# Kernel tuning notes

Hardware: AMD Instinct MI355X
Metric: run time of the kernel (lower is better)

## Reference

```python
import jax, jax.numpy as jnp
import numpy as np


def gat(feat_src, feat_dst, src, dst, W, al, ar, b):
    # DGL GATConv in eval mode: shared fc for src/dst, additive attention,
    # leaky_relu(0.2), edge-softmax per destination node, elu activation, bias.
    H, D = al.shape
    nd = feat_dst.shape[0]
    hs = (feat_src @ W).reshape(-1, H, D)  # [Ns,H,D]
    hd = (feat_dst @ W).reshape(-1, H, D)  # [Nd,H,D]
    el = (hs * al).sum(-1)  # [Ns,H]
    er = (hd * ar).sum(-1)  # [Nd,H]
    e = jax.nn.leaky_relu(el[src] + er[dst], 0.2)  # [E,H]
    m = jax.lax.stop_gradient(jax.ops.segment_max(e, dst, num_segments=nd))
    a = jnp.exp(e - m[dst])
    s = jax.ops.segment_sum(a, dst, num_segments=nd)
    den = s[dst]
    alpha = a / jnp.where(den == 0, 1.0, den)  # allow_zero_in_degree
    rst = jax.ops.segment_sum(alpha[:, :, None] * hs[src], dst, num_segments=nd)
    return jax.nn.elu(rst + b.reshape(H, D))  # [Nd,H,D]


def setup_inputs():
    key = jax.random.key(0)
    ks = jax.random.split(key, 40)
    NP, NQ, NK, NA = 50000, 20000, 30000, 5000
    EM, EQ, EK, EA = 1600000, 200000, 200000, 100000
    IN, ATT, HID, H, OUT = 128, 64, 32, 4, 1000
    w = lambda k, sh: jax.random.normal(k, sh, jnp.float32) * 0.05
    ri = lambda k, e, n: jax.random.randint(k, (e,), 0, n, dtype=jnp.int32)
    d = dict(
        hp=jax.random.normal(ks[0], (NP, IN), jnp.float32),
        hq=jax.random.normal(ks[1], (NQ, ATT), jnp.float32),
        hk=jax.random.normal(ks[2], (NK, ATT), jnp.float32),
        ha=jax.random.normal(ks[3], (NA, ATT), jnp.float32),
        meta_src=ri(ks[4], EM, NP), meta_dst=ri(ks[5], EM, NP),
        q_src=ri(ks[6], EQ, NQ), q_dst=ri(ks[7], EQ, NP),
        k_src=ri(ks[8], EK, NK), k_dst=ri(ks[9], EK, NP),
        a_src=ri(ks[10], EA, NA), a_dst=ri(ks[11], EA, NP),
        W0=w(ks[12], (IN, H * HID)), al0=w(ks[13], (H, HID)), ar0=w(ks[14], (H, HID)), b0=jnp.zeros((H * HID,), jnp.float32),
        W1=w(ks[15], (H * HID, H * HID)), al1=w(ks[16], (H, HID)), ar1=w(ks[17], (H, HID)), b1=jnp.zeros((H * HID,), jnp.float32),
        Wq=w(ks[18], (64, H * 128)), alq=w(ks[19], (H, 128)), arq=w(ks[20], (H, 128)), bq=jnp.zeros((H * 128,), jnp.float32),
        Wkw=w(ks[21], (64, H * 128)), alkw=w(ks[22], (H, 128)), arkw=w(ks[23], (H, 128)), bkw=jnp.zeros((H * 128,), jnp.float32),
        Watt=w(ks[24], (64, H * 128)), alatt=w(ks[25], (H, 128)), aratt=w(ks[26], (H, 128)), batt=jnp.zeros((H * 128,), jnp.float32),
        Wpnn_a=w(ks[27], (IN, 64)), Wpn_a=w(ks[28], (ATT, 64)),
        Wpnn=w(ks[29], (H * HID, 64)), Wpn=w(ks[30], (H * 128, 64)),
        Wpred=w(ks[31], (256, OUT)), bpred=jnp.zeros((OUT,), jnp.float32),
    )
    return d


def reference(hp, hq, hk, ha, meta_src, meta_dst, q_src, q_dst, k_src, k_dst, a_src, a_dst, W0, al0, ar0, b0, W1, al1, ar1, b1, Wq, alq, arq, bq, Wkw, alkw, arkw, bkw, Watt, alatt, aratt, batt, Wpnn_a, Wpn_a, Wpnn, Wpn, Wpred, bpred):
    NP = hp.shape[0]
    # two pnn_layers over the single used metapath graph (index 1 is skipped in the original)
    h = gat(hp, hp, meta_src, meta_dst, W0, al0, ar0, b0).reshape(NP, -1)  # [NP,128]
    h = gat(h, h, meta_src, meta_dst, W1, al1, ar1, b1).reshape(NP, -1)    # [NP,128]
    hpd = hp @ Wpnn_a  # proj_pnn_a(hp_cache) -> dst features for bipartite GATs
    oq = gat(hq @ Wpn_a, hpd, q_src, q_dst, Wq, alq, arq, bq).reshape(NP, -1)      # [NP,512]
    ok = gat(hk @ Wpn_a, hpd, k_src, k_dst, Wkw, alkw, arkw, bkw).reshape(NP, -1)  # [NP,512]
    oa = gat(ha @ Wpn_a, hpd, a_src, a_dst, Watt, alatt, aratt, batt).reshape(NP, -1)  # [NP,512]
    hcat = jnp.concatenate([h @ Wpnn, oq @ Wpn, ok @ Wpn, oa @ Wpn], axis=1)  # [NP,256]
    return hcat @ Wpred + bpred
```

## Files before the change

### kernel.cpp

```cpp
#include <hip/hip_runtime.h>
#include <hip/hip_bf16.h>
#include <math.h>
#include <stdint.h>

typedef __attribute__((ext_vector_type(8))) short bh8;
typedef __attribute__((ext_vector_type(4))) float f32x4;

#define AS1(p) ((const __attribute__((address_space(1))) void*)(p))
#define AS3(p) ((__attribute__((address_space(3))) void*)(p))
#define PSL 2048

__device__ inline ushort f2b(float f){
  uint u = __builtin_bit_cast(uint, f);
  u += 0x7fff + ((u >> 16) & 1);
  return (ushort)(u >> 16);
}
__device__ inline float b2f(ushort b){ return __builtin_bit_cast(float, (uint)b << 16); }

__global__ void fill_zero_i32(int* __restrict__ p, int n){
  int i = blockIdx.x*blockDim.x + threadIdx.x;
  if(i < n) p[i] = 0;
}

struct P4 { const int* src; const int* dst; uint* ebuf; int E; int cap; int bbeg; int bend; };

__global__ __launch_bounds__(256) void partition_all_k(P4 g0, P4 g1, P4 g2, P4 g3,
    int* __restrict__ bcur, int range){
  P4 G; int gi;
  int b = blockIdx.x;
  if(b < g0.bend){ G = g0; gi = 0; }
  else if(b < g1.bend){ G = g1; gi = 1; }
  else if(b < g2.bend){ G = g2; gi = 2; }
  else { G = g3; gi = 3; }
  const int beg = (b - G.bbeg)*PSL;
  const int tid = threadIdx.x, w = tid >> 6;
  __shared__ int hist4[4][8];
  __shared__ int cur4[4][8];
  if(tid < 32) (&hist4[0][0])[tid] = 0;
  __syncthreads();
  int dv[8], sv[8], bv[8];
  const int bi = beg + tid*8;
  if(beg + PSL <= G.E){
    int4 d0 = *(const int4*)(G.dst + bi);
    int4 d1 = *(const int4*)(G.dst + bi + 4);
    int4 s0 = *(const int4*)(G.src + bi);
    int4 s1 = *(const int4*)(G.src + bi + 4);
    dv[0]=d0.x; dv[1]=d0.y; dv[2]=d0.z; dv[3]=d0.w;
    dv[4]=d1.x; dv[5]=d1.y; dv[6]=d1.z; dv[7]=d1.w;
    sv[0]=s0.x; sv[1]=s0.y; sv[2]=s0.z; sv[3]=s0.w;
    sv[4]=s1.x; sv[5]=s1.y; sv[6]=s1.z; sv[7]=s1.w;
    #pragma unroll
    for(int u = 0; u < 8; u++) bv[u] = dv[u]/range;
  } else {
    #pragma unroll
    for(int u = 0; u < 8; u++){
      int i = bi + u;
      bool ok = i < G.E;
      dv[u] = ok ? G.dst[i] : 0;
      sv[u] = ok ? G.src[i] : 0;
      bv[u] = ok ? dv[u]/range : -1;
    }
  }
  #pragma unroll
  for(int u = 0; u < 8; u++) if(bv[u] >= 0) atomicAdd(&hist4[w][bv[u]], 1);
  __syncthreads();
  if(tid < 8){
    int h0 = hist4[0][tid], h1 = hist4[1][tid], h2 = hist4[2][tid], h3 = hist4[3][tid];
    int tot = h0 + h1 + h2 + h3;
    int bs = tot ? atomicAdd(&bcur[(gi*8 + tid)*16], tot) : 0;
    cur4[0][tid] = bs;
    cur4[1][tid] = bs + h0;
    cur4[2][tid] = bs + h0 + h1;
    cur4[3][tid] = bs + h0 + h1 + h2;
  }
  __syncthreads();
  #pragma unroll
  for(int u = 0; u < 8; u++) if(bv[u] >= 0){
    int pos = atomicAdd(&cur4[w][bv[u]], 1);
    if(pos < G.cap) G.ebuf[(size_t)bv[u]*G.cap + pos] = ((uint)sv[u] << 13) | (uint)(dv[u] - bv[u]*range);
  }
}

struct H4 { const uint* ebuf; int cap; };
__global__ __launch_bounds__(256) void hist_all_k(H4 h0, H4 h1, H4 h2, H4 h3,
    const int* __restrict__ bcur, int* __restrict__ part,
    int range, int NPL, int J, int NP){
  __shared__ int h[8192];
  const int x = blockIdx.x;
  const int g = x/(8*J);
  const int rem = x - g*8*J;
  const int bk = rem/J, j = rem - bk*J;
  H4 H = g==0 ? h0 : (g==1 ? h1 : (g==2 ? h2 : h3));
  for(int i = threadIdx.x; i < range; i += 256) h[i] = 0;
  __syncthreads();
  int nb = bcur[(g*8 + bk)*16]; if(nb > H.cap) nb = H.cap;
  const uint* eb = H.ebuf + (size_t)bk*H.cap;
  int per = (nb + J - 1)/J;
  int lo = j*per, hi = lo + per; if(hi > nb) hi = nb;
  for(int i = lo + threadIdx.x; i < hi; i += 256)
    atomicAdd(&h[eb[i] & 8191u], 1);
  __syncthreads();
  int lim = NP - bk*range; if(lim > range) lim = range;
  int* dst = part + ((size_t)g*J + j)*NPL + bk*range;
  for(int i = threadIdx.x; i < lim; i += 256) dst[i] = h[i];
}

struct SB4 { const uint* ebuf; int cap; int* cursor; int* colv; int bbeg; int bend; };
__global__ __launch_bounds__(256) void scatter_all_k(SB4 g0, SB4 g1, SB4 g2, SB4 g3,
    const int* __restrict__ bcur, int range){
  SB4 G; int gi;
  int b = blockIdx.x;
  if(b < g0.bend){ G = g0; gi = 0; }
  else if(b < g1.bend){ G = g1; gi = 1; }
  else if(b < g2.bend){ G = g2; gi = 2; }
  else { G = g3; gi = 3; }
  const int local = b - G.bbeg, J = (G.bend - G.bbeg) >> 3;
  const int bk = local & 7, j = local >> 3;
  int nb = bcur[(gi*8 + bk)*16]; if(nb > G.cap) nb = G.cap;
  const uint* eb = G.ebuf + (size_t)bk*G.cap;
  int* ub = G.cursor + bk*range;
  int per = (nb + J - 1)/J;
  int beg = j*per, end = beg + per; if(end > nb) end = nb;
  for(int i = beg + threadIdx.x; i < end; i += 256){
    uint e = eb[i];
    int p = atomicAdd(&ub[e & 8191u], 1);
    G.colv[p] = (int)(e >> 13);
  }
}

__global__ __launch_bounds__(1024) void scan4_k(
    const int* __restrict__ part, int J, int NPL,
    int* o0, int* o1, int* o2, int* o3,
    int* u0, int* u1, int* u2, int* u3, int n){
  const int* pg = part + (size_t)blockIdx.x*J*NPL;
  int* ofs    = blockIdx.x==0?o0:(blockIdx.x==1?o1:(blockIdx.x==2?o2:o3));
  int* cursor = blockIdx.x==0?u0:(blockIdx.x==1?u1:(blockIdx.x==2?u2:u3));
  __shared__ int wsum[16];
  __shared__ int carry_s;
  int tid = threadIdx.x, wid = tid >> 6, lane = tid & 63;
  if(tid == 0) carry_s = 0;
  __syncthreads();
  for(int base = 0; base < n; base += 4096){
    int i0 = base + tid*4;
    int4 v = make_int4(0,0,0,0);
    if(i0 + 3 < n){
      for(int j = 0; j < J; j++){
        int4 t = *(const int4*)(pg + (size_t)j*NPL + i0);
        v.x += t.x; v.y += t.y; v.z += t.z; v.w += t.w;
      }
    } else if(i0 < n){
      for(int j = 0; j < J; j++){
        v.x += pg[(size_t)j*NPL + i0];
        if(i0+1 < n) v.y += pg[(size_t)j*NPL + i0+1];
        if(i0+2 < n) v.z += pg[(size_t)j*NPL + i0+2];
      }
    }
    int s1 = v.x + v.y, s2 = s1 + v.z, tot = s2 + v.w;
    int x = tot;
    #pragma unroll
    for(int off = 1; off < 64; off <<= 1){
      int t = __shfl_up(x, off);
      if(lane >= off) x += t;
    }
    if(lane == 63) wsum[wid] = x;
    __syncthreads();
    if(tid < 16){
      int y = wsum[tid];
      #pragma unroll
      for(int off = 1; off < 16; off <<= 1){
        int t = __shfl_up(y, off);
        if(tid >= off) y += t;
      }
      wsum[tid] = y;
    }
    __syncthreads();
    int pre = (wid ? wsum[wid-1] : 0) + carry_s + (x - tot);
    if(i0 + 3 < n){
      int4 o = make_int4(pre, pre+v.x, pre+s1, pre+s2);
      *(int4*)(ofs + i0) = o;
      *(int4*)(cursor + i0) = o;
    } else if(i0 < n){
      ofs[i0] = pre; cursor[i0] = pre;
      if(i0+1 < n){ ofs[i0+1] = pre+v.x; cursor[i0+1] = pre+v.x; }
      if(i0+2 < n){ ofs[i0+2] = pre+s1; cursor[i0+2] = pre+s1; }
    }
    __syncthreads();
    if(tid == 0) carry_s += wsum[15];
    __syncthreads();
  }
  if(tid == 0) ofs[n] = carry_s;
}

__global__ void cvt_all_k(const float* i0, const float* i1, const float* i2, const float* i3,
    ushort* o0, ushort* o1, ushort* o2, ushort* o3, int4 cum){
  int i = blockIdx.x*blockDim.x + threadIdx.x;
  const float* in; ushort* out; int base;
  if(i < cum.x){ in=i0; out=o0; base=0; }
  else if(i < cum.y){ in=i1; out=o1; base=cum.x; }
  else if(i < cum.z){ in=i2; out=o2; base=cum.y; }
  else if(i < cum.w){ in=i3; out=o3; base=cum.z; }
  else return;
  int l = i - base;
  float4 v = ((const float4*)in)[l];
  ushort4 o; o.x=f2b(v.x); o.y=f2b(v.y); o.z=f2b(v.z); o.w=f2b(v.w);
  ((ushort4*)out)[l] = o;
}

struct WTD { const float* W; ushort* WT; int K; int N; };
struct WTAll { WTD d[7]; int cum[8]; };
__global__ void wT_all_k(WTAll a){
  int idx = blockIdx.x*blockDim.x + threadIdx.x;
  if(idx >= a.cum[7]) return;
  int j = 0;
  #pragma unroll
  for(int t = 1; t < 7; t++) if(idx >= a.cum[t]) j = t;
  int l = idx - a.cum[j];
  WTD d = a.d[j];
  int n = l / d.K, k = l - n*d.K;
  d.WT[l] = (n < d.N) ? f2b(d.W[(size_t)k*d.N + n]) : (ushort)0;
}

__global__ void wTg3_k(const float* W0, const float* W1, const float* W2, ushort* WT){
  int idx = blockIdx.x*blockDim.x + threadIdx.x;
  if(idx >= 3*32768) return;
  int g = idx >> 15, rem = idx & 32767;
  const float* W = g==0 ? W0 : (g==1 ? W1 : W2);
  int h = rem >> 13, r2 = rem & 8191;
  int n = r2 >> 6, k = r2 & 63;
  WT[idx] = f2b(W[(size_t)k*512 + h*128 + n]);
}

struct FD { const float* W; const float* a; float* out; int K; int D; };
struct FAll { FD d[10]; };
__global__ void fold_all_k(FAll f){
  FD d = f.d[blockIdx.x];
  for(int i = threadIdx.x; i < d.K*4; i += 256){
    int k = i >> 2, h = i & 3;
    const float* wr = d.W + (size_t)k*4*d.D + (size_t)h*d.D;
    const float* ar = d.a + (size_t)h*d.D;
    float s = 0.f;
    for(int dd = 0; dd < d.D; dd++) s += wr[dd]*ar[dd];
    d.out[i] = s;
  }
}

__device__ inline void ld4v(const float* p, float* v){
  float4 t = *(const float4*)p; v[0]=t.x; v[1]=t.y; v[2]=t.z; v[3]=t.w;
}
__device__ inline void ld4v(const ushort* p, float* v){
  ushort4 t = *(const ushort4*)p; v[0]=b2f(t.x); v[1]=b2f(t.y); v[2]=b2f(t.z); v[3]=b2f(t.w);
}

__global__ __launch_bounds__(256) void gemv4v_seg3(const ushort* __restrict__ A,
    const float* __restrict__ W0, const float* __restrict__ W1, const float* __restrict__ W2,
    float* __restrict__ outv, int M, int b1, int b2){
  const int w = (blockIdx.x*blockDim.x + threadIdx.x) >> 6;
  const int lane = threadIdx.x & 63;
  const int r = lane >> 4, q = lane & 15;
  int row = w*4 + r;
  bool valid = row < M;
  int rowc = valid ? row : (M-1);
  const float* Wf = rowc < b1 ? W0 : (rowc < b2 ? W1 : W2);
  float av[4];
  ld4v(A + (size_t)rowc*64 + q*4, av);
  float a[4] = {0.f,0.f,0.f,0.f};
  #pragma unroll
  for(int kk = 0; kk < 4; kk++){
    float4 wv = *(const float4*)(Wf + (q*4+kk)*4);
    a[0] += av[kk]*wv.x; a[1] += av[kk]*wv.y; a[2] += av[kk]*wv.z; a[3] += av[kk]*wv.w;
  }
  #pragma unroll
  for(int off = 1; off < 16; off <<= 1){
    a[0] += __shfl_xor(a[0], off); a[1] += __shfl_xor(a[1], off);
    a[2] += __shfl_xor(a[2], off); a[3] += __shfl_xor(a[3], off);
  }
  if(valid && q == 0){
    float4 o; o.x=a[0]; o.y=a[1]; o.z=a[2]; o.w=a[3];
    *(float4*)(outv + (size_t)row*4) = o;
  }
}

__global__ __launch_bounds__(256) void gemv4v_er3(const ushort* __restrict__ A,
    const float* __restrict__ W0, const float* __restrict__ W1, const float* __restrict__ W2,
    float* __restrict__ o0, float* __restrict__ o1, float* __restrict__ o2, int M){
  const int w = (blockIdx.x*blockDim.x + threadIdx.x) >> 6;
  const int lane = threadIdx.x & 63;
  const int r = lane >> 4, q = lane & 15;
  int row = w*4 + r;
  bool valid = row < M;
  int rowc = valid ? row : (M-1);
  float av[4];
  ld4v(A + (size_t)rowc*64 + q*4, av);
  float a[12];
  #pragma unroll
  for(int t = 0; t < 12; t++) a[t] = 0.f;
  #pragma unroll
  for(int kk = 0; kk < 4; kk++){
    float4 w0 = *(const float4*)(W0 + (q*4+kk)*4);
    float4 w1 = *(const float4*)(W1 + (q*4+kk)*4);
    float4 w2 = *(const float4*)(W2 + (q*4+kk)*4);
    a[0] += av[kk]*w0.x; a[1] += av[kk]*w0.y; a[2] += av[kk]*w0.z; a[3] += av[kk]*w0.w;
    a[4] += av[kk]*w1.x; a[5] += av[kk]*w1.y; a[6] += av[kk]*w1.z; a[7] += av[kk]*w1.w;
    a[8] += av[kk]*w2.x; a[9] += av[kk]*w2.y; a[10]+= av[kk]*w2.z; a[11]+= av[kk]*w2.w;
  }
  #pragma unroll
  for(int off = 1; off < 16; off <<= 1)
    #pragma unroll
    for(int t = 0; t < 12; t++) a[t] += __shfl_xor(a[t], off);
  if(valid && q == 0){
    float4 x; x.x=a[0]; x.y=a[1]; x.z=a[2]; x.w=a[3];
    *(float4*)(o0 + (size_t)row*4) = x;
    float4 y; y.x=a[4]; y.y=a[5]; y.z=a[6]; y.w=a[7];
    *(float4*)(o1 + (size_t)row*4) = y;
    float4 z; z.x=a[8]; z.y=a[9]; z.z=a[10]; z.w=a[11];
    *(float4*)(o2 + (size_t)row*4) = z;
  }
}

template<typename T>
__global__ __launch_bounds__(256) void gemv8v(const T* __restrict__ A,
    const float* __restrict__ Wfa, const float* __restrict__ Wfb,
    float* __restrict__ oa, float* __restrict__ ob, int M, int lda){
  const int w = (blockIdx.x*blockDim.x + threadIdx.x) >> 6;
  const int lane = threadIdx.x & 63;
  const int r = lane >> 5, q = lane & 31;
  int row = w*2 + r;
  bool valid = row < M;
  int rowc = valid ? row : (M-1);
  float av[4];
  ld4v(A + (size_t)rowc*lda + q*4, av);
  float a[4] = {0.f,0.f,0.f,0.f}, b[4] = {0.f,0.f,0.f,0.f};
  #pragma unroll
  for(int kk = 0; kk < 4; kk++){
    float4 wa = *(const float4*)(Wfa + (q*4+kk)*4);
    float4 wb = *(const float4*)(Wfb + (q*4+kk)*4);
    a[0] += av[kk]*wa.x; a[1] += av[kk]*wa.y; a[2] += av[kk]*wa.z; a[3] += av[kk]*wa.w;
    b[0] += av[kk]*wb.x; b[1] += av[kk]*wb.y; b[2] += av[kk]*wb.z; b[3] += av[kk]*wb.w;
  }
  #pragma unroll
  for(int off = 1; off < 32; off <<= 1){
    a[0] += __shfl_xor(a[0], off); a[1] += __shfl_xor(a[1], off);
    a[2] += __shfl_xor(a[2], off); a[3] += __shfl_xor(a[3], off);
    b[0] += __shfl_xor(b[0], off); b[1] += __shfl_xor(b[1], off);
    b[2] += __shfl_xor(b[2], off); b[3] += __shfl_xor(b[3], off);
  }
  if(valid && q == 0){
    float4 o; o.x=a[0]; o.y=a[1]; o.z=a[2]; o.w=a[3];
    *(float4*)(oa + (size_t)row*4) = o;
    float4 p; p.x=b[0]; p.y=b[1]; p.z=b[2]; p.w=b[3];
    *(float4*)(ob + (size_t)row*4) = p;
  }
}

struct GSeg { const ushort* A; const ushort* BT; const float* bias; void* C; int ldc; };

template<int BN, typename OutT, bool BIAS>
__global__ __launch_bounds__(256) void gemm_mfma_b(GSeg s0, GSeg s1, GSeg s2,
    int M, int N, int K, int lda){
  constexpr int BM = 128, BK = 64;
  constexpr int NI = BN/32;
  constexpr int AIT = BM*BK/(256*8);
  constexpr int BIT = BN*BK/(256*8);
  __shared__ ushort lds[BM*BK + BN*BK];
  ushort* ldsA = lds;
  ushort* ldsB = lds + BM*BK;
  GSeg S = blockIdx.z == 0 ? s0 : (blockIdx.z == 1 ? s1 : s2);
  const int tid = threadIdx.x, wid = tid >> 6, lane = tid & 63;
  const int wr = wid >> 1, wc = wid & 1;
  const int rowbase = blockIdx.x*BM;
  const int colbase = blockIdx.y*BN;

  f32x4 acc[4][NI];
  #pragma unroll
  for(int mi = 0; mi < 4; mi++)
    #pragma unroll
    for(int ni = 0; ni < NI; ni++) acc[mi][ni] = (f32x4)0.f;

  for(int k0 = 0; k0 < K; k0 += BK){
    #pragma unroll
    for(int it = 0; it < AIT; it++){
      int idx = it*256 + wid*64 + lane;
      int r = idx >> 3, sl = idx & 7;
      int kb = sl ^ (r & 7);
      int grow = rowbase + r; if(grow >= M) grow = M-1;
      const ushort* src = S.A + (size_t)grow*lda + k0 + kb*8;
      __builtin_amdgcn_global_load_lds(AS1(src), AS3(ldsA + (size_t)(it*256 + wid*64)*8), 16, 0, 0);
    }
    #pragma unroll
    for(int it = 0; it < BIT; it++){
      int idx = it*256 + wid*64 + lane;
      int r = idx >> 3, sl = idx & 7;
      int kb = sl ^ (r & 7);
      const ushort* src = S.BT + (size_t)(colbase + r)*K + k0 + kb*8;
      __builtin_amdgcn_global_load_lds(AS1(src), AS3(ldsB + (size_t)(it*256 + wid*64)*8), 16, 0, 0);
    }
    __syncthreads();
    #pragma unroll
    for(int kk = 0; kk < 2; kk++){
      bh8 af[4], bf[NI];
      #pragma unroll
      for(int mi = 0; mi < 4; mi++){
        int arow = wr*64 + mi*16 + (lane & 15);
        int kb = kk*4 + (lane >> 4);
        af[mi] = *(const bh8*)(ldsA + arow*BK + ((kb ^ (arow & 7)) << 3));
      }
      #pragma unroll
      for(int ni = 0; ni < NI; ni++){
        int brow = wc*(BN/2) + ni*16 + (lane & 15);
        int kb = kk*4 + (lane >> 4);
        bf[ni] = *(const bh8*)(ldsB + brow*BK + ((kb ^ (brow & 7)) << 3));
      }
      #pragma unroll
      for(int mi = 0; mi < 4; mi++)
        #pragma unroll
        for(int ni = 0; ni < NI; ni++)
          acc[mi][ni] = __builtin_amdgcn_mfma_f32_16x16x32_bf16(af[mi], bf[ni], acc[mi][ni], 0, 0, 0);
    }
    __syncthreads();
  }
  OutT* C = (OutT*)S.C;
  #pragma unroll
  for(int mi = 0; mi < 4; mi++){
    #pragma unroll
    for(int ni = 0; ni < NI; ni++){
      int col = colbase + wc*(BN/2) + ni*16 + (lane & 15);
      if(col >= N) continue;
      float bv = BIAS ? S.bias[col] : 0.f;
      #pragma unroll
      for(int j = 0; j < 4; j++){
        int row = rowbase + wr*64 + mi*16 + (lane >> 4)*4 + j;
        if(row >= M) continue;
        float v = acc[mi][ni][j] + bv;
        if constexpr (sizeof(OutT) == 4) C[(size_t)row*S.ldc + col] = v;
        else                             C[(size_t)row*S.ldc + col] = (OutT)f2b(v);
      }
    }
  }
}

__global__ __launch_bounds__(256) void bip_tail_k(
    const ushort* __restrict__ agg, const ushort* __restrict__ WTg3,
    const ushort* __restrict__ WpnT,
    const float* bias0, const float* bias1, const float* bias2,
    ushort* __restrict__ hcat, int M){
  __shared__ ushort ldsA[128*64];
  __shared__ ushort ldsB[128*64];
  __shared__ ushort ldsP[128*128];
  __shared__ ushort ldsW[64*128];
  const int seg = blockIdx.z;
  const ushort* A  = agg + (size_t)seg*M*256;
  const ushort* Wg = WTg3 + (size_t)seg*32768;
  const float* bias = seg==0 ? bias0 : (seg==1 ? bias1 : bias2);
  ushort* outp = hcat + 64 + seg*64;
  const int tid = threadIdx.x, lane = tid & 63, wid = tid >> 6;
  const int wr = wid >> 1, wc = wid & 1;
  const int rowbase = blockIdx.x*128;

  f32x4 acc_out[4][2];
  #pragma unroll
  for(int mi = 0; mi < 4; mi++){ acc_out[mi][0] = (f32x4)0.f; acc_out[mi][1] = (f32x4)0.f; }

  for(int hh = 0; hh < 4; hh++){
    #pragma unroll
    for(int it = 0; it < 4; it++){
      int idx = it*256 + tid;
      int r = idx >> 3, sl = idx & 7;
      int kb = sl ^ (r & 7);
      int grow = rowbase + r; if(grow >= M) grow = M-1;
      __builtin_amdgcn_global_load_lds(AS1(A + (size_t)grow*256 + hh*64 + kb*8),
                                       AS3(ldsA + (size_t)idx*8), 16, 0, 0);
    }
    #pragma unroll
    for(int it = 0; it < 4; it++){
      int idx = it*256 + tid;
      int r = idx >> 3, sl = idx & 7;
      int kb = sl ^ (r & 7);
      __builtin_amdgcn_global_load_lds(AS1(Wg + hh*8192 + r*64 + kb*8),
                                       AS3(ldsB + (size_t)idx*8), 16, 0, 0);
    }
    #pragma unroll
    for(int it = 0; it < 4; it++){
      int idx = it*256 + tid;
      int r = idx >> 4, sl = idx & 15;
      int kb = sl ^ (r & 7);
      __builtin_amdgcn_global_load_lds(AS1(WpnT + (size_t)r*512 + hh*128 + kb*8),
                                       AS3(ldsW + (size_t)idx*8), 16, 0, 0);
    }
    __syncthreads();
    f32x4 accp[4][4];
    #pragma unroll
    for(int mi = 0; mi < 4; mi++)
      #pragma unroll
      for(int ni = 0; ni < 4; ni++) accp[mi][ni] = (f32x4)0.f;
    #pragma unroll
    for(int kk = 0; kk < 2; kk++){
      bh8 af[4], bf[4];
      int kb = kk*4 + (lane >> 4);
      #pragma unroll
      for(int mi = 0; mi < 4; mi++){
        int arow = wr*64 + mi*16 + (lane & 15);
        af[mi] = *(const bh8*)(ldsA + arow*64 + ((kb ^ (arow & 7)) << 3));
      }
      #pragma unroll
      for(int ni = 0; ni < 4; ni++){
        int brow = wc*64 + ni*16 + (lane & 15);
        bf[ni] = *(const bh8*)(ldsB + brow*64 + ((kb ^ (brow & 7)) << 3));
      }
      #pragma unroll
      for(int mi = 0; mi < 4; mi++)
        #pragma unroll
        for(int ni = 0; ni < 4; ni++)
          accp[mi][ni] = __builtin_amdgcn_mfma_f32_16x16x32_bf16(af[mi], bf[ni], accp[mi][ni], 0, 0, 0);
    }
    #pragma unroll
    for(int mi = 0; mi < 4; mi++)
      #pragma unroll
      for(int ni = 0; ni < 4; ni++){
        int col = wc*64 + ni*16 + (lane & 15);
        float bv = bias[hh*128 + col];
        int rbase = wr*64 + mi*16 + (lane >> 4)*4;
        #pragma unroll
        for(int j = 0; j < 4; j++){
          float v = accp[mi][ni][j] + bv;
          v = v > 0.f ? v : (__expf(v) - 1.f);
          int row = rbase + j;
          ldsP[row*128 + ((((col >> 3) ^ (row & 7))) << 3) + (col & 7)] = f2b(v);
        }
      }
    __syncthreads();
    #pragma unroll
    for(int kk = 0; kk < 4; kk++){
      bh8 af[4], bf[2];
      int kb = kk*4 + (lane >> 4);
      #pragma unroll
      for(int mi = 0; mi < 4; mi++){
        int arow = wr*64 + mi*16 + (lane & 15);
        af[mi] = *(const bh8*)(ldsP + arow*128 + ((kb ^ (arow & 7)) << 3));
      }
      #pragma unroll
      for(int ni = 0; ni < 2; ni++){
        int brow = wc*32 + ni*16 + (lane & 15);
        bf[ni] = *(const bh8*)(ldsW + brow*128 + ((kb ^ (brow & 7)) << 3));
      }
      #pragma unroll
      for(int mi = 0; mi < 4; mi++)
        #pragma unroll
        for(int ni = 0; ni < 2; ni++)
          acc_out[mi][ni] = __builtin_amdgcn_mfma_f32_16x16x32_bf16(af[mi], bf[ni], acc_out[mi][ni], 0, 0, 0);
    }
    __syncthreads();
  }
  #pragma unroll
  for(int mi = 0; mi < 4; mi++)
    #pragma unroll
    for(int ni = 0; ni < 2; ni++){
      int col = wc*32 + ni*16 + (lane & 15);
      #pragma unroll
      for(int j = 0; j < 4; j++){
        int row = rowbase + wr*64 + mi*16 + (lane >> 4)*4 + j;
        if(row >= M) continue;
        outp[(size_t)row*256 + col] = f2b(acc_out[mi][ni][j]);
      }
    }
}

__global__ __launch_bounds__(256) void gat_agg_meta(
    const ushort* __restrict__ hs, const float* __restrict__ el,
    const float* __restrict__ er, const int* __restrict__ ofs,
    const int* __restrict__ colv, const float* __restrict__ bias,
    ushort* __restrict__ outv, int Nd){
  const int wslot = threadIdx.x >> 6;
  const int node = blockIdx.x*4 + wslot;
  const int lane = threadIdx.x & 63;
  __shared__ int   lds_s[4][64];
  __shared__ float lds_w[4][256];
  if(node >= Nd) return;
  const int e0 = ofs[node], e1 = ofs[node+1];
  const int g = lane >> 4, q = lane & 15;
  const int hh = q >> 2;
  const float4 erv = *(const float4*)(er + (size_t)node*4);
  float m0=-INFINITY, m1=-INFINITY, m2=-INFINITY, m3=-INFINITY;
  float sw0=0.f, sw1=0.f, sw2=0.f, sw3=0.f;
  float acc[8];
  #pragma unroll
  for(int r = 0; r < 8; r++) acc[r] = 0.f;

  for(int base = e0; base < e1; base += 64){
    int nch = e1 - base; if(nch > 64) nch = 64;
    int s_l = colv[base + (lane < nch ? lane : nch-1)];
    float4 ev = *(const float4*)(el + (size_t)s_l*4);
    float x0 = ev.x + erv.x; x0 = x0 > 0.f ? x0 : 0.2f*x0;
    float x1 = ev.y + erv.y; x1 = x1 > 0.f ? x1 : 0.2f*x1;
    float x2 = ev.z + erv.z; x2 = x2 > 0.f ? x2 : 0.2f*x2;
    float x3 = ev.w + erv.w; x3 = x3 > 0.f ? x3 : 0.2f*x3;
    if(lane >= nch){ x0 = x1 = x2 = x3 = -INFINITY; }
    float c0=x0, c1=x1, c2=x2, c3=x3;
    #pragma unroll
    for(int off = 32; off; off >>= 1){
      c0 = fmaxf(c0, __shfl_xor(c0, off));
      c1 = fmaxf(c1, __shfl_xor(c1, off));
      c2 = fmaxf(c2, __shfl_xor(c2, off));
      c3 = fmaxf(c3, __shfl_xor(c3, off));
    }
    float n0 = fmaxf(m0,c0), n1 = fmaxf(m1,c1), n2 = fmaxf(m2,c2), n3 = fmaxf(m3,c3);
    float r0 = __expf(m0-n0), r1 = __expf(m1-n1), r2 = __expf(m2-n2), r3 = __expf(m3-n3);
    float w0 = __expf(x0-n0), w1 = __expf(x1-n1), w2 = __expf(x2-n2), w3 = __expf(x3-n3);
    sw0 = sw0*r0 + w0; sw1 = sw1*r1 + w1; sw2 = sw2*r2 + w2; sw3 = sw3*r3 + w3;
    float rh = hh==0 ? r0 : (hh==1 ? r1 : (hh==2 ? r2 : r3));
    #pragma unroll
    for(int r = 0; r < 8; r++) acc[r] *= rh;
    m0=n0; m1=n1; m2=n2; m3=n3;
    lds_s[wslot][lane] = s_l;
    lds_w[wslot][lane*4+0] = w0; lds_w[wslot][lane*4+1] = w1;
    lds_w[wslot][lane*4+2] = w2; lds_w[wslot][lane*4+3] = w3;
    int npad = (nch + 15) & ~15;
    for(int j = 0; j < npad; j += 16){
      int sv[4]; float wv[4];
      #pragma unroll
      for(int u = 0; u < 4; u++){
        sv[u] = lds_s[wslot][j + u*4 + g];
        wv[u] = lds_w[wslot][(j + u*4 + g)*4 + hh];
      }
      bh8 vv[4];
      #pragma unroll
      for(int u = 0; u < 4; u++)
        vv[u] = *(const bh8*)(hs + (size_t)sv[u]*128 + q*8);
      #pragma unroll
      for(int u = 0; u < 4; u++)
        #pragma unroll
        for(int r = 0; r < 8; r++) acc[r] += wv[u] * b2f((ushort)vv[u][r]);
    }
  }
  #pragma unroll
  for(int off = 32; off; off >>= 1){
    sw0 += __shfl_xor(sw0, off); sw1 += __shfl_xor(sw1, off);
    sw2 += __shfl_xor(sw2, off); sw3 += __shfl_xor(sw3, off);
  }
  #pragma unroll
  for(int r = 0; r < 8; r++){
    acc[r] += __shfl_xor(acc[r], 16);
    acc[r] += __shfl_xor(acc[r], 32);
  }
  float swh = hh==0 ? sw0 : (hh==1 ? sw1 : (hh==2 ? sw2 : sw3));
  float den = (swh == 0.f) ? 1.f : swh;
  if(g == 0){
    bh8 ov;
    #pragma unroll
    for(int r = 0; r < 8; r++){
      float v = acc[r]/den + bias[q*8 + r];
      v = v > 0.f ? v : (__expf(v) - 1.f);
      ov[r] = (short)f2b(v);
    }
    *(bh8*)(outv + (size_t)node*128 + q*8) = ov;
  }
}

struct ASeg { const int* ofs; const int* colv; const float* el; const float* er; ushort* agg; };
__global__ __launch_bounds__(256) void gat_agg_proj3(ASeg s0, ASeg s1, ASeg s2,
    const ushort* __restrict__ proj, int2 pbase, int Nd, int nb){
  const int seg = blockIdx.x / nb;
  const ASeg S = seg == 0 ? s0 : (seg == 1 ? s1 : s2);
  const ushort* pj = proj + (size_t)(seg == 0 ? 0 : (seg == 1 ? pbase.x : pbase.y))*64;
  const int node = (blockIdx.x - seg*nb)*16 + (threadIdx.x >> 4);
  const int q = threadIdx.x & 15;
  if(node >= Nd) return;
  const int e0 = S.ofs[node], e1 = S.ofs[node+1];
  const int deg = e1 - e0;
  const float4 erv = *(const float4*)(S.er + (size_t)node*4);
  float sw0=0.f, sw1=0.f, sw2=0.f, sw3=0.f;
  float acc[4][4];
  #pragma unroll
  for(int d = 0; d < 4; d++)
    #pragma unroll
    for(int h = 0; h < 4; h++) acc[d][h] = 0.f;

  if(deg <= 8){
    const int ebase = (deg > 0) ? e0 : 0;
    int sv[8];
    #pragma unroll
    for(int u = 0; u < 8; u++) sv[u] = S.colv[ebase + (u < deg ? u : 0)];
    float xa[8], xb[8], xc[8], xd[8];
    #pragma unroll
    for(int u = 0; u < 8; u++){
      float4 ev = *(const float4*)(S.el + (size_t)sv[u]*4);
      float t0 = ev.x + erv.x; xa[u] = t0 > 0.f ? t0 : 0.2f*t0;
      float t1 = ev.y + erv.y; xb[u] = t1 > 0.f ? t1 : 0.2f*t1;
      float t2 = ev.z + erv.z; xc[u] = t2 > 0.f ? t2 : 0.2f*t2;
      float t3 = ev.w + erv.w; xd[u] = t3 > 0.f ? t3 : 0.2f*t3;
    }
    float m0=-INFINITY, m1=-INFINITY, m2=-INFINITY, m3=-INFINITY;
    #pragma unroll
    for(int u = 0; u < 8; u++) if(u < deg){
      m0 = fmaxf(m0, xa[u]); m1 = fmaxf(m1, xb[u]);
      m2 = fmaxf(m2, xc[u]); m3 = fmaxf(m3, xd[u]);
    }
    ushort4 pv[8];
    #pragma unroll
    for(int u = 0; u < 8; u++) pv[u] = *(const ushort4*)(pj + (size_t)sv[u]*64 + q*4);
    #pragma unroll
    for(int u = 0; u < 8; u++) if(u < deg){
      float w0 = __expf(xa[u]-m0), w1 = __expf(xb[u]-m1);
      float w2 = __expf(xc[u]-m2), w3 = __expf(xd[u]-m3);
      sw0 += w0; sw1 += w1; sw2 += w2; sw3 += w3;
      float f0 = b2f(pv[u].x), f1 = b2f(pv[u].y), f2 = b2f(pv[u].z), f3 = b2f(pv[u].w);
      acc[0][0] += w0*f0; acc[0][1] += w1*f0; acc[0][2] += w2*f0; acc[0][3] += w3*f0;
      acc[1][0] += w0*f1; acc[1][1] += w1*f1; acc[1][2] += w2*f1; acc[1][3] += w3*f1;
      acc[2][0] += w0*f2; acc[2][1] += w1*f2; acc[2][2] += w2*f2; acc[2][3] += w3*f2;
      acc[3][0] += w0*f3; acc[3][1] += w1*f3; acc[3][2] += w2*f3; acc[3][3] += w3*f3;
    }
  } else {
    float m0=-INFINITY, m1=-INFINITY, m2=-INFINITY, m3=-INFINITY;
    for(int e = e0; e < e1; e++){
      int s = S.colv[e];
      float4 ev = *(const float4*)(S.el + (size_t)s*4);
      float x0 = ev.x + erv.x; x0 = x0 > 0.f ? x0 : 0.2f*x0;
      float x1 = ev.y + erv.y; x1 = x1 > 0.f ? x1 : 0.2f*x1;
      float x2 = ev.z + erv.z; x2 = x2 > 0.f ? x2 : 0.2f*x2;
      float x3 = ev.w + erv.w; x3 = x3 > 0.f ? x3 : 0.2f*x3;
      m0 = fmaxf(m0,x0); m1 = fmaxf(m1,x1); m2 = fmaxf(m2,x2); m3 = fmaxf(m3,x3);
    }
    for(int e = e0; e < e1; e++){
      int s = S.colv[e];
      float4 ev = *(const float4*)(S.el + (size_t)s*4);
      float x0 = ev.x + erv.x; x0 = x0 > 0.f ? x0 : 0.2f*x0;
      float x1 = ev.y + erv.y; x1 = x1 > 0.f ? x1 : 0.2f*x1;
      float x2 = ev.z + erv.z; x2 = x2 > 0.f ? x2 : 0.2f*x2;
      float x3 = ev.w + erv.w; x3 = x3 > 0.f ? x3 : 0.2f*x3;
      float w0 = __expf(x0-m0), w1 = __expf(x1-m1);
      float w2 = __expf(x2-m2), w3 = __expf(x3-m3);
      sw0 += w0; sw1 += w1; sw2 += w2; sw3 += w3;
      ushort4 p = *(const ushort4*)(pj + (size_t)s*64 + q*4);
      float f0 = b2f(p.x), f1 = b2f(p.y), f2 = b2f(p.z), f3 = b2f(p.w);
      acc[0][0] += w0*f0; acc[0][1] += w1*f0; acc[0][2] += w2*f0; acc[0][3] += w3*f0;
      acc[1][0] += w0*f1; acc[1][1] += w1*f1; acc[1][2] += w2*f1; acc[1][3] += w3*f1;
      acc[2][0] += w0*f2; acc[2][1] += w1*f2; acc[2][2] += w2*f2; acc[2][3] += w3*f2;
      acc[3][0] += w0*f3; acc[3][1] += w1*f3; acc[3][2] += w2*f3; acc[3][3] += w3*f3;
    }
  }
  float dn[4];
  dn[0] = (sw0 == 0.f) ? 1.f : sw0;
  dn[1] = (sw1 == 0.f) ? 1.f : sw1;
  dn[2] = (sw2 == 0.f) ? 1.f : sw2;
  dn[3] = (sw3 == 0.f) ? 1.f : sw3;
  ushort* orow = S.agg + (size_t)node*256;
  #pragma unroll
  for(int h = 0; h < 4; h++){
    ushort4 o;
    o.x = f2b(acc[0][h]/dn[h]); o.y = f2b(acc[1][h]/dn[h]);
    o.z = f2b(acc[2][h]/dn[h]); o.w = f2b(acc[3][h]/dn[h]);
    *(ushort4*)(orow + h*64 + q*4) = o;
  }
}

extern "C" void kernel_launch(void* const* d_in, const int* in_sizes, int n_in,
                              void* d_out, int out_size, void* d_ws, size_t ws_size,
                              hipStream_t stream){
  const float* hp   = (const float*)d_in[0];
  const float* hq   = (const float*)d_in[1];
  const float* hk   = (const float*)d_in[2];
  const float* ha   = (const float*)d_in[3];
  const int* meta_src = (const int*)d_in[4];
  const int* meta_dst = (const int*)d_in[5];
  const int* q_src = (const int*)d_in[6];
  const int* q_dst = (const int*)d_in[7];
  const int* k_src = (const int*)d_in[8];
  const int* k_dst = (const int*)d_in[9];
  const int* a_src = (const int*)d_in[10];
  const int* a_dst = (const int*)d_in[11];
  const float* W0  = (const float*)d_in[12]; const float* al0 = (const float*)d_in[13];
  const float* ar0 = (const float*)d_in[14]; const float* b0  = (const float*)d_in[15];
  const float* W1  = (const float*)d_in[16]; const float* al1 = (const float*)d_in[17];
  const float* ar1 = (const float*)d_in[18]; const float* b1  = (const float*)d_in[19];
  const float* Wq  = (const float*)d_in[20]; const float* alq = (const float*)d_in[21];
  const float* arq = (const float*)d_in[22]; const float* bq  = (const float*)d_in[23];
  const float* Wkw = (const float*)d_in[24]; const float* alkw= (const float*)d_in[25];
  const float* arkw= (const float*)d_in[26]; const float* bkw = (const float*)d_in[27];
  const float* Watt= (const float*)d_in[28]; const float* alatt=(const float*)d_in[29];
  const float* aratt=(const float*)d_in[30]; const float* batt= (const float*)d_in[31];
  const float* Wpnn_a = (const float*)d_in[32];
  const float* Wpn_a  = (const float*)d_in[33];
  const float* Wpnn   = (const float*)d_in[34];
  const float* Wpn    = (const float*)d_in[35];
  const float* Wpred  = (const float*)d_in[36];
  const float* bpred  = (const float*)d_in[37];
  (void)n_in; (void)out_size; (void)ws_size;

  const int IN = 128, ATT = 64;
  const int NP = in_sizes[0]/IN, NQ = in_sizes[1]/ATT, NK = in_sizes[2]/ATT, NA = in_sizes[3]/ATT;
  const int EM = in_sizes[4], EQ = in_sizes[6], EK = in_sizes[8], EA = in_sizes[10];
  const int range = (NP + 7)/8;
  const int NS = NQ + NK + NA;
  const int JH = 8;
  const int NPL = (NP + 3) & ~3;

  uint8_t* wp = (uint8_t*)d_ws;
  auto alloc = [&](size_t bytes)->uint8_t*{
    uint8_t* p = wp; wp += (bytes + 255) & ~(size_t)255; return p;
  };
  ushort* hcat_b = (ushort*)alloc((size_t)NP*256*2);
  ushort* hbuf_b = (ushort*)alloc((size_t)NP*128*2);
  ushort* hp_b   = (ushort*)alloc((size_t)NP*128*2);
  ushort* hpd_b  = (ushort*)alloc((size_t)NP*64*2);
  ushort* hs_b   = (ushort*)alloc((size_t)NP*128*2);
  ushort* feat_all = (ushort*)alloc((size_t)NS*64*2);
  ushort* proj_all = (ushort*)alloc((size_t)NS*64*2);
  ushort* agg_all  = (ushort*)alloc((size_t)3*NP*256*2);
  float* el    = (float*)alloc((size_t)NP*4*4);
  float* er    = (float*)alloc((size_t)NP*4*4);
  float* el_all= (float*)alloc((size_t)NS*4*4);
  float* er_all= (float*)alloc((size_t)3*NP*4*4);
  float* wf    = (float*)alloc((size_t)10*512*4);
  int* bcur    = (int*)alloc((size_t)512*4);
  int* part    = (int*)alloc((size_t)4*JH*NPL*4);
  int* cur4    = (int*)alloc((size_t)4*NP*4);
  int* ofsm    = (int*)alloc((size_t)(NP+4)*4);
  int* ofsq    = (int*)alloc((size_t)(NP+4)*4);
  int* ofsk    = (int*)alloc((size_t)(NP+4)*4);
  int* ofsa    = (int*)alloc((size_t)(NP+4)*4);
  int* colm    = (int*)alloc((size_t)EM*4);
  int* colq    = (int*)alloc((size_t)EQ*4);
  int* colk    = (int*)alloc((size_t)EK*4);
  int* cola    = (int*)alloc((size_t)EA*4);
  const int capM = EM/4+1024, capQ = EQ/4+1024, capK = EK/4+1024, capA = EA/4+1024;
  uint* ebm = (uint*)alloc((size_t)8*capM*4);
  uint* ebq = (uint*)alloc((size_t)8*capQ*4);
  uint* ebk = (uint*)alloc((size_t)8*capK*4);
  uint* eba = (uint*)alloc((size_t)8*capA*4);
  ushort* W0T    = (ushort*)alloc(128*128*2);
  ushort* W1T    = (ushort*)alloc(128*128*2);
  ushort* WTg3   = (ushort*)alloc((size_t)3*4*128*64*2);
  ushort* WpnT   = (ushort*)alloc((size_t)64*512*2);
  ushort* WpnnT  = (ushort*)alloc(64*128*2);
  ushort* Wpnn_aT= (ushort*)alloc(64*128*2);
  ushort* Wpn_aT = (ushort*)alloc(64*64*2);
  ushort* WpredT = (ushort*)alloc((size_t)1024*256*2);

  fill_zero_i32<<<2, 256, 0, stream>>>(bcur, 512);
  {
    int bm = (EM+PSL-1)/PSL, bq2 = (EQ+PSL-1)/PSL, bk2 = (EK+PSL-1)/PSL, ba2 = (EA+PSL-1)/PSL;
    P4 g0{meta_src, meta_dst, ebm, EM, capM, 0, bm};
    P4 g1{q_src, q_dst, ebq, EQ, capQ, bm, bm+bq2};
    P4 g2{k_src, k_dst, ebk, EK, capK, bm+bq2, bm+bq2+bk2};
    P4 g3{a_src, a_dst, eba, EA, capA, bm+bq2+bk2, bm+bq2+bk2+ba2};
    partition_all_k<<<g3.bend, 256, 0, stream>>>(g0, g1, g2, g3, bcur, range);
  }
  {
    H4 h0{ebm, capM}, h1{ebq, capQ}, h2{ebk, capK}, h3{eba, capA};
    hist_all_k<<<4*8*JH, 256, 0, stream>>>(h0, h1, h2, h3, bcur, part, range, NPL, JH, NP);
    scan4_k<<<4, 1024, 0, stream>>>(part, JH, NPL,
                                    ofsm, ofsq, ofsk, ofsa,
                                    cur4, cur4+NP, cur4+2*NP, cur4+3*NP, NP);
    auto Jof = [&](int E){ int J = E/65536 + 8; if(J > 48) J = 48; return J; };
    int jm = 8*Jof(EM), jq = 8*Jof(EQ), jk = 8*Jof(EK), ja = 8*Jof(EA);
    SB4 s0{ebm, capM, cur4 + 0*NP, colm, 0, jm};
    SB4 s1{ebq, capQ, cur4 + 1*NP, colq, jm, jm+jq};
    SB4 s2{ebk, capK, cur4 + 2*NP, colk, jm+jq, jm+jq+jk};
    SB4 s3{eba, capA, cur4 + 3*NP, cola, jm+jq+jk, jm+jq+jk+ja};
    scatter_all_k<<<s3.bend, 256, 0, stream>>>(s0, s1, s2, s3, bcur, range);
  }

  {
    int c0 = NP*128/4, c1 = c0 + NQ*64/4, c2 = c1 + NK*64/4, c3 = c2 + NA*64/4;
    cvt_all_k<<<(c3+255)/256, 256, 0, stream>>>(hp, hq, hk, ha,
        hp_b, feat_all, feat_all + (size_t)NQ*64, feat_all + (size_t)(NQ+NK)*64,
        make_int4(c0, c1, c2, c3));
  }
  {
    WTAll a;
    a.d[0] = {W0, W0T, 128, 128};      a.d[1] = {W1, W1T, 128, 128};
    a.d[2] = {Wpn, WpnT, 512, 64};     a.d[3] = {Wpnn, WpnnT, 128, 64};
    a.d[4] = {Wpnn_a, Wpnn_aT, 128, 64}; a.d[5] = {Wpn_a, Wpn_aT, 64, 64};
    a.d[6] = {Wpred, WpredT, 256, 1000};
    int items[7] = {128*128, 128*128, 64*512, 64*128, 64*128, 64*64, 1024*256};
    a.cum[0] = 0;
    for(int t = 0; t < 7; t++) a.cum[t+1] = a.cum[t] + items[t];
    wT_all_k<<<(a.cum[7]+255)/256, 256, 0, stream>>>(a);
  }
  wTg3_k<<<(3*32768+255)/256, 256, 0, stream>>>(Wq, Wkw, Watt, WTg3);
  {
    FAll f;
    f.d[0] = {W0, al0, wf+0*512, 128, 32};  f.d[1] = {W0, ar0, wf+1*512, 128, 32};
    f.d[2] = {W1, al1, wf+2*512, 128, 32};  f.d[3] = {W1, ar1, wf+3*512, 128, 32};
    f.d[4] = {Wq, alq, wf+4*512, 64, 128};  f.d[5] = {Wq, arq, wf+5*512, 64, 128};
    f.d[6] = {Wkw, alkw, wf+6*512, 64, 128};f.d[7] = {Wkw, arkw, wf+7*512, 64, 128};
    f.d[8] = {Watt, alatt, wf+8*512, 64, 128};f.d[9] = {Watt, aratt, wf+9*512, 64, 128};
    fold_all_k<<<10, 256, 0, stream>>>(f);
  }

  auto launch_gemm = [&]<int BN, typename OutT, bool BIAS>(
      GSeg a, GSeg b, GSeg c, int nseg, int M, int N, int K, int lda){
    int Npad = (N + BN - 1)/BN*BN;
    dim3 g((M + 127)/128, Npad/BN, nseg);
    gemm_mfma_b<BN, OutT, BIAS><<<g, 256, 0, stream>>>(a, b, c, M, N, K, lda);
  };
  GSeg z{};

  launch_gemm.template operator()<128, ushort, false>(
      GSeg{hp_b, W0T, nullptr, hs_b, 128}, z, z, 1, NP, 128, 128, 128);
  gemv8v<ushort><<<(NP/2+3)/4, 256, 0, stream>>>(hp_b, wf+0*512, wf+1*512, el, er, NP, 128);
  gat_agg_meta<<<(NP+3)/4, 256, 0, stream>>>(hs_b, el, er, ofsm, colm, b0, hbuf_b, NP);

  launch_gemm.template operator()<128, ushort, false>(
      GSeg{hbuf_b, W1T, nullptr, hs_b, 128}, z, z, 1, NP, 128, 128, 128);
  gemv8v<ushort><<<(NP/2+3)/4, 256, 0, stream>>>(hbuf_b, wf+2*512, wf+3*512, el, er, NP, 128);
  gat_agg_meta<<<(NP+3)/4, 256, 0, stream>>>(hs_b, el, er, ofsm, colm, b1, hbuf_b, NP);

  launch_gemm.template operator()<64, ushort, false>(
      GSeg{hbuf_b, WpnnT, nullptr, hcat_b, 256},
      GSeg{hp_b, Wpnn_aT, nullptr, hpd_b, 64}, z, 2, NP, 64, 128, 128);

  launch_gemm.template operator()<64, ushort, false>(
      GSeg{feat_all, Wpn_aT, nullptr, proj_all, 64}, z, z, 1, NS, 64, 64, 64);
  gemv4v_seg3<<<(NS/4+3)/4, 256, 0, stream>>>(proj_all, wf+4*512, wf+6*512, wf+8*512,
      el_all, NS, NQ, NQ+NK);
  gemv4v_er3<<<(NP/4+3)/4, 256, 0, stream>>>(hpd_b, wf+5*512, wf+7*512, wf+9*512,
      er_all, er_all + (size_t)NP*4, er_all + (size_t)2*NP*4, NP);
  {
    int nb = (NP+15)/16;
    ASeg a0{ofsq, colq, el_all,                    er_all,                    agg_all};
    ASeg a1{ofsk, colk, el_all + (size_t)NQ*4,     er_all + (size_t)NP*4,     agg_all + (size_t)NP*256};
    ASeg a2{ofsa, cola, el_all + (size_t)(NQ+NK)*4,er_all + (size_t)2*NP*4,   agg_all + (size_t)2*NP*256};
    gat_agg_proj3<<<3*nb, 256, 0, stream>>>(a0, a1, a2, proj_all, make_int2(NQ, NQ+NK), NP, nb);
  }
  {
    dim3 g((NP+127)/128, 1, 3);
    bip_tail_k<<<g, 256, 0, stream>>>(agg_all, WTg3, WpnT, bq, bkw, batt, hcat_b, NP);
  }

  launch_gemm.template operator()<128, float, true>(
      GSeg{hcat_b, WpredT, bpred, d_out, 1000}, z, z, 1, NP, 1000, 256, 256);
}
```

Measured before the change: 715.5 us.

## Scatter edges with LDS cursors, merge projection GEMMs, unroll meta aggregation deeper

```diff
diff --git a/kernel.cpp b/kernel.cpp
--- a/kernel.cpp
+++ b/kernel.cpp
@@ -105,36 +105,40 @@
   for(int i = threadIdx.x; i < lim; i += 256) dst[i] = h[i];
 }
 
-struct SB4 { const uint* ebuf; int cap; int* cursor; int* colv; int bbeg; int bend; };
-__global__ __launch_bounds__(256) void scatter_all_k(SB4 g0, SB4 g1, SB4 g2, SB4 g3,
-    const int* __restrict__ bcur, int range){
-  SB4 G; int gi;
-  int b = blockIdx.x;
-  if(b < g0.bend){ G = g0; gi = 0; }
-  else if(b < g1.bend){ G = g1; gi = 1; }
-  else if(b < g2.bend){ G = g2; gi = 2; }
-  else { G = g3; gi = 3; }
-  const int local = b - G.bbeg, J = (G.bend - G.bbeg) >> 3;
-  const int bk = local & 7, j = local >> 3;
-  int nb = bcur[(gi*8 + bk)*16]; if(nb > G.cap) nb = G.cap;
+struct SC4 { const uint* ebuf; int cap; const int* ofs; int* colv; };
+__global__ __launch_bounds__(256) void scatter_lds_k(SC4 g0, SC4 g1, SC4 g2, SC4 g3,
+    const int* __restrict__ bcur, const int* __restrict__ part,
+    int range, int NPL, int J, int NP){
+  __shared__ int cur[8192];
+  const int x = blockIdx.x;
+  const int g = x/(8*J);
+  const int rem = x - g*8*J;
+  const int bk = rem/J, j = rem - bk*J;
+  SC4 G = g==0 ? g0 : (g==1 ? g1 : (g==2 ? g2 : g3));
+  int lim = NP - bk*range; if(lim > range) lim = range;
+  const int* pp = part + (size_t)g*J*NPL + bk*range;
+  for(int i = threadIdx.x; i < lim; i += 256){
+    int c = G.ofs[bk*range + i];
+    for(int jj = 0; jj < j; jj++) c += pp[(size_t)jj*NPL + i];
+    cur[i] = c;
+  }
+  __syncthreads();
+  int nb = bcur[(g*8 + bk)*16]; if(nb > G.cap) nb = G.cap;
   const uint* eb = G.ebuf + (size_t)bk*G.cap;
-  int* ub = G.cursor + bk*range;
   int per = (nb + J - 1)/J;
-  int beg = j*per, end = beg + per; if(end > nb) end = nb;
-  for(int i = beg + threadIdx.x; i < end; i += 256){
+  int lo = j*per, hi = lo + per; if(hi > nb) hi = nb;
+  for(int i = lo + threadIdx.x; i < hi; i += 256){
     uint e = eb[i];
-    int p = atomicAdd(&ub[e & 8191u], 1);
+    int p = atomicAdd(&cur[e & 8191u], 1);
     G.colv[p] = (int)(e >> 13);
   }
 }
 
 __global__ __launch_bounds__(1024) void scan4_k(
     const int* __restrict__ part, int J, int NPL,
-    int* o0, int* o1, int* o2, int* o3,
-    int* u0, int* u1, int* u2, int* u3, int n){
+    int* o0, int* o1, int* o2, int* o3, int n){
   const int* pg = part + (size_t)blockIdx.x*J*NPL;
-  int* ofs    = blockIdx.x==0?o0:(blockIdx.x==1?o1:(blockIdx.x==2?o2:o3));
-  int* cursor = blockIdx.x==0?u0:(blockIdx.x==1?u1:(blockIdx.x==2?u2:u3));
+  int* ofs = blockIdx.x==0?o0:(blockIdx.x==1?o1:(blockIdx.x==2?o2:o3));
   __shared__ int wsum[16];
   __shared__ int carry_s;
   int tid = threadIdx.x, wid = tid >> 6, lane = tid & 63;
@@ -176,13 +180,11 @@
     __syncthreads();
     int pre = (wid ? wsum[wid-1] : 0) + carry_s + (x - tot);
     if(i0 + 3 < n){
-      int4 o = make_int4(pre, pre+v.x, pre+s1, pre+s2);
-      *(int4*)(ofs + i0) = o;
-      *(int4*)(cursor + i0) = o;
+      *(int4*)(ofs + i0) = make_int4(pre, pre+v.x, pre+s1, pre+s2);
     } else if(i0 < n){
-      ofs[i0] = pre; cursor[i0] = pre;
-      if(i0+1 < n){ ofs[i0+1] = pre+v.x; cursor[i0+1] = pre+v.x; }
-      if(i0+2 < n){ ofs[i0+2] = pre+s1; cursor[i0+2] = pre+s1; }
+      ofs[i0] = pre;
+      if(i0+1 < n) ofs[i0+1] = pre+v.x;
+      if(i0+2 < n) ofs[i0+2] = pre+s1;
     }
     __syncthreads();
     if(tid == 0) carry_s += wsum[15];
@@ -352,11 +354,10 @@
   }
 }
 
-struct GSeg { const ushort* A; const ushort* BT; const float* bias; void* C; int ldc; };
+struct GSeg { const ushort* A; const ushort* BT; const float* bias; void* C; int ldc; int M; int K; int lda; };
 
 template<int BN, typename OutT, bool BIAS>
-__global__ __launch_bounds__(256) void gemm_mfma_b(GSeg s0, GSeg s1, GSeg s2,
-    int M, int N, int K, int lda){
+__global__ __launch_bounds__(256) void gemm_mfma_b(GSeg s0, GSeg s1, GSeg s2, int N){
   constexpr int BM = 128, BK = 64;
   constexpr int NI = BN/32;
   constexpr int AIT = BM*BK/(256*8);
@@ -365,9 +366,10 @@
   ushort* ldsA = lds;
   ushort* ldsB = lds + BM*BK;
   GSeg S = blockIdx.z == 0 ? s0 : (blockIdx.z == 1 ? s1 : s2);
+  const int rowbase = blockIdx.x*BM;
+  if(rowbase >= S.M) return;
   const int tid = threadIdx.x, wid = tid >> 6, lane = tid & 63;
   const int wr = wid >> 1, wc = wid & 1;
-  const int rowbase = blockIdx.x*BM;
   const int colbase = blockIdx.y*BN;
 
   f32x4 acc[4][NI];
@@ -376,14 +378,14 @@
     #pragma unroll
     for(int ni = 0; ni < NI; ni++) acc[mi][ni] = (f32x4)0.f;
 
-  for(int k0 = 0; k0 < K; k0 += BK){
+  for(int k0 = 0; k0 < S.K; k0 += BK){
     #pragma unroll
     for(int it = 0; it < AIT; it++){
       int idx = it*256 + wid*64 + lane;
       int r = idx >> 3, sl = idx & 7;
       int kb = sl ^ (r & 7);
-      int grow = rowbase + r; if(grow >= M) grow = M-1;
-      const ushort* src = S.A + (size_t)grow*lda + k0 + kb*8;
+      int grow = rowbase + r; if(grow >= S.M) grow = S.M-1;
+      const ushort* src = S.A + (size_t)grow*S.lda + k0 + kb*8;
       __builtin_amdgcn_global_load_lds(AS1(src), AS3(ldsA + (size_t)(it*256 + wid*64)*8), 16, 0, 0);
     }
     #pragma unroll
@@ -391,7 +393,7 @@
       int idx = it*256 + wid*64 + lane;
       int r = idx >> 3, sl = idx & 7;
       int kb = sl ^ (r & 7);
-      const ushort* src = S.BT + (size_t)(colbase + r)*K + k0 + kb*8;
+      const ushort* src = S.BT + (size_t)(colbase + r)*S.K + k0 + kb*8;
       __builtin_amdgcn_global_load_lds(AS1(src), AS3(ldsB + (size_t)(it*256 + wid*64)*8), 16, 0, 0);
     }
     __syncthreads();
@@ -429,7 +431,7 @@
       #pragma unroll
       for(int j = 0; j < 4; j++){
         int row = rowbase + wr*64 + mi*16 + (lane >> 4)*4 + j;
-        if(row >= M) continue;
+        if(row >= S.M) continue;
         float v = acc[mi][ni][j] + bv;
         if constexpr (sizeof(OutT) == 4) C[(size_t)row*S.ldc + col] = v;
         else                             C[(size_t)row*S.ldc + col] = (OutT)f2b(v);
@@ -613,20 +615,20 @@
     lds_s[wslot][lane] = s_l;
     lds_w[wslot][lane*4+0] = w0; lds_w[wslot][lane*4+1] = w1;
     lds_w[wslot][lane*4+2] = w2; lds_w[wslot][lane*4+3] = w3;
-    int npad = (nch + 15) & ~15;
-    for(int j = 0; j < npad; j += 16){
-      int sv[4]; float wv[4];
-      #pragma unroll
-      for(int u = 0; u < 4; u++){
+    int npad = (nch + 31) & ~31;
+    for(int j = 0; j < npad; j += 32){
+      int sv[8]; float wv[8];
+      #pragma unroll
+      for(int u = 0; u < 8; u++){
         sv[u] = lds_s[wslot][j + u*4 + g];
         wv[u] = lds_w[wslot][(j + u*4 + g)*4 + hh];
       }
-      bh8 vv[4];
-      #pragma unroll
-      for(int u = 0; u < 4; u++)
+      bh8 vv[8];
+      #pragma unroll
+      for(int u = 0; u < 8; u++)
         vv[u] = *(const bh8*)(hs + (size_t)sv[u]*128 + q*8);
       #pragma unroll
-      for(int u = 0; u < 4; u++)
+      for(int u = 0; u < 8; u++)
         #pragma unroll
         for(int r = 0; r < 8; r++) acc[r] += wv[u] * b2f((ushort)vv[u][r]);
     }
@@ -812,7 +814,6 @@
   float* wf    = (float*)alloc((size_t)10*512*4);
   int* bcur    = (int*)alloc((size_t)512*4);
   int* part    = (int*)alloc((size_t)4*JH*NPL*4);
-  int* cur4    = (int*)alloc((size_t)4*NP*4);
   int* ofsm    = (int*)alloc((size_t)(NP+4)*4);
   int* ofsq    = (int*)alloc((size_t)(NP+4)*4);
   int* ofsk    = (int*)alloc((size_t)(NP+4)*4);
@@ -847,16 +848,12 @@
   {
     H4 h0{ebm, capM}, h1{ebq, capQ}, h2{ebk, capK}, h3{eba, capA};
     hist_all_k<<<4*8*JH, 256, 0, stream>>>(h0, h1, h2, h3, bcur, part, range, NPL, JH, NP);
-    scan4_k<<<4, 1024, 0, stream>>>(part, JH, NPL,
-                                    ofsm, ofsq, ofsk, ofsa,
-                                    cur4, cur4+NP, cur4+2*NP, cur4+3*NP, NP);
-    auto Jof = [&](int E){ int J = E/65536 + 8; if(J > 48) J = 48; return J; };
-    int jm = 8*Jof(EM), jq = 8*Jof(EQ), jk = 8*Jof(EK), ja = 8*Jof(EA);
-    SB4 s0{ebm, capM, cur4 + 0*NP, colm, 0, jm};
-    SB4 s1{ebq, capQ, cur4 + 1*NP, colq, jm, jm+jq};
-    SB4 s2{ebk, capK, cur4 + 2*NP, colk, jm+jq, jm+jq+jk};
-    SB4 s3{eba, capA, cur4 + 3*NP, cola, jm+jq+jk, jm+jq+jk+ja};
-    scatter_all_k<<<s3.bend, 256, 0, stream>>>(s0, s1, s2, s3, bcur, range);
+    scan4_k<<<4, 1024, 0, stream>>>(part, JH, NPL, ofsm, ofsq, ofsk, ofsa, NP);
+    SC4 s0{ebm, capM, ofsm, colm};
+    SC4 s1{ebq, capQ, ofsq, colq};
+    SC4 s2{ebk, capK, ofsk, colk};
+    SC4 s3{eba, capA, ofsa, cola};
+    scatter_lds_k<<<4*8*JH, 256, 0, stream>>>(s0, s1, s2, s3, bcur, part, range, NPL, JH, NP);
   }
 
   {
@@ -888,29 +885,28 @@
   }
 
   auto launch_gemm = [&]<int BN, typename OutT, bool BIAS>(
-      GSeg a, GSeg b, GSeg c, int nseg, int M, int N, int K, int lda){
+      GSeg a, GSeg b, GSeg c, int nseg, int maxM, int N){
     int Npad = (N + BN - 1)/BN*BN;
-    dim3 g((M + 127)/128, Npad/BN, nseg);
-    gemm_mfma_b<BN, OutT, BIAS><<<g, 256, 0, stream>>>(a, b, c, M, N, K, lda);
+    dim3 g((maxM + 127)/128, Npad/BN, nseg);
+    gemm_mfma_b<BN, OutT, BIAS><<<g, 256, 0, stream>>>(a, b, c, N);
   };
   GSeg z{};
 
   launch_gemm.template operator()<128, ushort, false>(
-      GSeg{hp_b, W0T, nullptr, hs_b, 128}, z, z, 1, NP, 128, 128, 128);
+      GSeg{hp_b, W0T, nullptr, hs_b, 128, NP, 128, 128}, z, z, 1, NP, 128);
   gemv8v<ushort><<<(NP/2+3)/4, 256, 0, stream>>>(hp_b, wf+0*512, wf+1*512, el, er, NP, 128);
   gat_agg_meta<<<(NP+3)/4, 256, 0, stream>>>(hs_b, el, er, ofsm, colm, b0, hbuf_b, NP);
 
   launch_gemm.template operator()<128, ushort, false>(
-      GSeg{hbuf_b, W1T, nullptr, hs_b, 128}, z, z, 1, NP, 128, 128, 128);
+      GSeg{hbuf_b, W1T, nullptr, hs_b, 128, NP, 128, 128}, z, z, 1, NP, 128);
   gemv8v<ushort><<<(NP/2+3)/4, 256, 0, stream>>>(hbuf_b, wf+2*512, wf+3*512, el, er, NP, 128);
   gat_agg_meta<<<(NP+3)/4, 256, 0, stream>>>(hs_b, el, er, ofsm, colm, b1, hbuf_b, NP);
 
   launch_gemm.template operator()<64, ushort, false>(
-      GSeg{hbuf_b, WpnnT, nullptr, hcat_b, 256},
-      GSeg{hp_b, Wpnn_aT, nullptr, hpd_b, 64}, z, 2, NP, 64, 128, 128);
-
-  launch_gemm.template operator()<64, ushort, false>(
-      GSeg{feat_all, Wpn_aT, nullptr, proj_all, 64}, z, z, 1, NS, 64, 64, 64);
+      GSeg{feat_all, Wpn_aT, nullptr, proj_all, 64, NS, 64, 64},
+      GSeg{hbuf_b, WpnnT, nullptr, hcat_b, 256, NP, 128, 128},
+      GSeg{hp_b, Wpnn_aT, nullptr, hpd_b, 64, NP, 128, 128}, 3, NS > NP ? NS : NP, 64);
+
   gemv4v_seg3<<<(NS/4+3)/4, 256, 0, stream>>>(proj_all, wf+4*512, wf+6*512, wf+8*512,
       el_all, NS, NQ, NQ+NK);
   gemv4v_er3<<<(NP/4+3)/4, 256, 0, stream>>>(hpd_b, wf+5*512, wf+7*512, wf+9*512,
@@ -928,5 +924,5 @@
   }
 
   launch_gemm.template operator()<128, float, true>(
-      GSeg{hcat_b, WpredT, bpred, d_out, 1000}, z, z, 1, NP, 1000, 256, 256);
-}
+      GSeg{hcat_b, WpredT, bpred, d_out, 1000, NP, 256, 256}, z, z, 1, NP, 1000);
+}
```

Measured after the change: 713.6 us. Within noise of the previous version (-0.3%).
